# Performance work log

Measured on AMD Instinct MI355X. Metric: run time of the kernel, lower is better.

Reference implementation:

```python
import jax, jax.numpy as jnp
import numpy as np

N_NODES = 100000
N_EDGES = 1600000
N_GRAPHS = 64
VOCAB = 50000
D = 128
EPS = 1e-5


def setup_inputs() -> dict:
    key = jax.random.key(0)
    ks = jax.random.split(key, 24)
    tokens = jax.random.randint(ks[0], (N_NODES,), 0, VOCAB)
    src = jax.random.randint(ks[1], (N_EDGES,), 0, N_NODES)
    dst = jax.random.randint(ks[2], (N_EDGES,), 0, N_NODES)
    graph_ids = jnp.sort(jax.random.randint(ks[3], (N_NODES,), 0, N_GRAPHS))
    s = 1.0 / np.sqrt(D)
    inp = {
        'tokens': tokens, 'src': src, 'dst': dst, 'graph_ids': graph_ids,
        'embed': jax.random.normal(ks[4], (VOCAB, D), jnp.float32),
        'W1': jax.random.normal(ks[5], (D, D), jnp.float32) * s,
        'b1': jnp.zeros((D,), jnp.float32),
        'g1': jnp.ones((D,), jnp.float32), 'be1': jnp.zeros((D,), jnp.float32),
        'W2': jax.random.normal(ks[6], (D, D), jnp.float32) * s,
        'b2': jnp.zeros((D,), jnp.float32),
        'g2': jnp.ones((D,), jnp.float32), 'be2': jnp.zeros((D,), jnp.float32),
        'W3': jax.random.normal(ks[7], (D, D), jnp.float32) * s,
        'b3': jnp.zeros((D,), jnp.float32),
        'g3': jnp.ones((D,), jnp.float32), 'be3': jnp.zeros((D,), jnp.float32),
        'fcW1': jax.random.normal(ks[8], (D, D // 2), jnp.float32) * s,
        'fcb1': jnp.zeros((D // 2,), jnp.float32),
        'fcW2': jax.random.normal(ks[9], (D // 2, 2), jnp.float32) * (1.0 / np.sqrt(D // 2)),
        'fcb2': jnp.zeros((2,), jnp.float32),
    }
    return inp


def _graph_conv(h, src, dst, norm_src, norm_dst, W, b):
    # DGL GraphConv, norm='both': D_out^{-1/2} -> sum-aggregate -> D_in^{-1/2} -> linear
    msg = (h * norm_src[:, None])[src]                      # [E, D]
    agg = jax.ops.segment_sum(msg, dst, num_segments=N_NODES)
    return (agg * norm_dst[:, None]) @ W + b


def _bn_relu(h, gamma, beta):
    mu = jnp.mean(h, axis=0)
    var = jnp.mean((h - mu) ** 2, axis=0)                   # biased var (torch BN)
    return jax.nn.relu((h - mu) * jax.lax.rsqrt(var + EPS) * gamma + beta)


def reference(tokens, src, dst, graph_ids, embed,
              W1, b1, g1, be1, W2, b2, g2, be2, W3, b3, g3, be3,
              fcW1, fcb1, fcW2, fcb2):
    ones_e = jnp.ones((N_EDGES,), jnp.float32)
    deg_out = jnp.maximum(jax.ops.segment_sum(ones_e, src, num_segments=N_NODES), 1.0)
    deg_in = jnp.maximum(jax.ops.segment_sum(ones_e, dst, num_segments=N_NODES), 1.0)
    norm_src = jax.lax.rsqrt(deg_out)
    norm_dst = jax.lax.rsqrt(deg_in)

    h = embed[tokens]                                        # [N, D]
    h = _bn_relu(_graph_conv(h, src, dst, norm_src, norm_dst, W1, b1), g1, be1)
    h = _bn_relu(_graph_conv(h, src, dst, norm_src, norm_dst, W2, b2), g2, be2)
    h = _bn_relu(_graph_conv(h, src, dst, norm_src, norm_dst, W3, b3), g3, be3)

    # dgl.mean_nodes per graph
    sums = jax.ops.segment_sum(h, graph_ids, num_segments=N_GRAPHS)  # [G, D]
    cnts = jnp.maximum(jax.ops.segment_sum(jnp.ones((N_NODES,), jnp.float32), graph_ids, num_segments=N_GRAPHS), 1.0)
    hg = sums / cnts[:, None]

    hg = jax.nn.relu(hg @ fcW1 + fcb1)                       # dropout = identity (eval)
    return hg @ fcW2 + fcb2                                  # [G, 2]
```

## Files before the change

### kernel.cpp

```cpp
#include <hip/hip_runtime.h>

#define N_NODES 100000
#define N_EDGES 1600000
#define N_GRAPHS 64
#define DIM 128
#define BN_EPS 1e-5f
#define EPAD 2000000

#define NB_SENT 977
#define NB_WPREP 192
#define NB_HIST 391
#define NB_ZERO 40
#define NBUCK 782
#define NG (NBUCK * NB_HIST)
#define NB_SCANG 1195
#define BUCK_RESERVE 388

#define AT_STRIDE 136

typedef unsigned short ushort_t;
typedef unsigned char uchar_t;
typedef unsigned int uint_t;
typedef __attribute__((ext_vector_type(8))) short bf16x8;
typedef __attribute__((ext_vector_type(4))) float f32x4;

__device__ __forceinline__ float bfl(uint_t u) {
    union { uint_t i; float f; } v; v.i = u << 16; return v.f;
}
__device__ __forceinline__ float bfh(uint_t u) {
    union { uint_t i; float f; } v; v.i = u & 0xffff0000u; return v.f;
}
__device__ __forceinline__ ushort_t f2bf(float f) {
    union { float f; uint_t i; } v; v.f = f;
    uint_t x = v.i;
    return (ushort_t)((x + 0x7fffu + ((x >> 16) & 1u)) >> 16);
}
__device__ __forceinline__ uint_t pack2(float lo, float hi) {
    return ((uint_t)f2bf(hi) << 16) | (uint_t)f2bf(lo);
}

__global__ void k_front(const int* __restrict__ src, const int* __restrict__ dst,
                        ushort_t* __restrict__ bufA, int* __restrict__ esrc,
                        const float* __restrict__ w1, const float* __restrict__ w2,
                        const float* __restrict__ w3, ushort_t* __restrict__ wbt,
                        int* __restrict__ GG, int* __restrict__ deg,
                        int* __restrict__ zp, int zwords) {
    __shared__ int hh[NBUCK];
    int b = blockIdx.x;
    int t = threadIdx.x;
    if (b < NB_SENT) {
        int i0 = (b * 256 + t) * 8;
        int4 sv = make_int4(N_NODES, N_NODES, N_NODES, N_NODES);
        if (i0 + 8 <= EPAD) {
            *(int4*)(esrc + i0) = sv;
            *(int4*)(esrc + i0 + 4) = sv;
        } else {
            for (int i = i0; i < EPAD; ++i) esrc[i] = N_NODES;
        }
        if (b == 0 && t < 64)
            ((uint_t*)(bufA + (size_t)N_NODES * DIM))[t] = 0u;
        return;
    }
    b -= NB_SENT;
    if (b < NB_WPREP) {
        int i = b * 256 + t;
        int l = i >> 14;
        int idx = i & (DIM * DIM - 1);
        int n = idx >> 7, k = idx & (DIM - 1);
        const float* wsrc = (l == 0) ? w1 : (l == 1) ? w2 : w3;
        wbt[i] = f2bf(wsrc[k * DIM + n]);
        return;
    }
    b -= NB_WPREP;
    if (b < NB_HIST) {
        for (int k = t; k < NBUCK; k += 256) hh[k] = 0;
        __syncthreads();
        int e0 = b * 4096;
        int e1 = min(e0 + 4096, N_EDGES);
        for (int i = e0 + t; i < e1; i += 256) {
            atomicAdd(&hh[dst[i] >> 7], 1);
            atomicAdd(&deg[src[i]], 1);
        }
        __syncthreads();
        for (int k = t; k < NBUCK; k += 256)
            GG[k * NB_HIST + b] = hh[k];
        return;
    }
    b -= NB_HIST;
    {
        int i = b * 256 + t;
        if (i < zwords) zp[i] = 0;
    }
}

__global__ void k_scanA(const int* __restrict__ GG, int* __restrict__ Gs,
                        int* __restrict__ partials) {
    __shared__ int s[256];
    int t = threadIdx.x;
    int i = blockIdx.x * 256 + t;
    int v = (i < NG) ? GG[i] : 0;
    s[t] = v;
    __syncthreads();
    for (int off = 1; off < 256; off <<= 1) {
        int add = (t >= off) ? s[t - off] : 0;
        __syncthreads();
        s[t] += add;
        __syncthreads();
    }
    if (i < NG) Gs[i + 1] = s[t];
    if (t == 255) partials[blockIdx.x] = s[t];
}

__global__ void k_scanB(const int* __restrict__ partials, int* __restrict__ Gs) {
    __shared__ int s[256];
    int t = threadIdx.x;
    int p = 0;
    for (int j = t; j < (int)blockIdx.x; j += 256) p += partials[j];
    s[t] = p;
    __syncthreads();
    for (int off = 128; off > 0; off >>= 1) {
        if (t < off) s[t] += s[t + off];
        __syncthreads();
    }
    int prefix = s[0];
    int i = blockIdx.x * 256 + t;
    if (i < NG) Gs[i + 1] += prefix;
    if (blockIdx.x == 0 && t == 0) Gs[0] = 0;
}

__global__ void k_pass2(const int* __restrict__ src, const int* __restrict__ dst,
                        const int* __restrict__ Gs, uint_t* __restrict__ Cpk) {
    __shared__ int cur[NBUCK];
    int b = blockIdx.x;
    int t = threadIdx.x;
    for (int k = t; k < NBUCK; k += 256)
        cur[k] = Gs[k * NB_HIST + b];
    __syncthreads();
    int e0 = b * 4096;
    int e1 = min(e0 + 4096, N_EDGES);
    for (int i = e0 + t; i < e1; i += 256) {
        int d = dst[i];
        int s = src[i];
        int slot = atomicAdd(&cur[d >> 7], 1);
        Cpk[slot] = (uint_t)s | ((uint_t)(d & 127) << 17);
    }
}

__global__ void k_fine(const uint_t* __restrict__ Cpk, const int* __restrict__ Gs,
                       const int* __restrict__ deg,
                       const int* __restrict__ tokens, const float* __restrict__ embed,
                       int* __restrict__ esrc, int* __restrict__ rowptr,
                       int* __restrict__ pdeg, float* __restrict__ ns,
                       float* __restrict__ nd, ushort_t* __restrict__ bufA) {
    __shared__ int hcnt[128];
    __shared__ int hstart[128];
    __shared__ float lns[128];
    int k = blockIdx.x;
    int t = threadIdx.x;
    int node0 = k * 128;
    int nn = min(128, N_NODES - node0);
    int S = Gs[k * NB_HIST];
    int E = Gs[(k + 1) * NB_HIST];
    if (t < 128) hcnt[t] = 0;
    __syncthreads();
    for (int i = S + t; i < E; i += 256) atomicAdd(&hcnt[Cpk[i] >> 17], 1);
    __syncthreads();
    if (t == 0) {
        int acc = 0;
        for (int n = 0; n < nn; ++n) {
            hstart[n] = acc;
            acc += (hcnt[n] + 3) & ~3;
        }
    }
    __syncthreads();
    int base = (k * BUCK_RESERVE + S + 3) & ~3;
    if (t < nn) {
        int node = node0 + t;
        rowptr[node] = base + hstart[t];
        pdeg[node] = (hcnt[t] + 3) & ~3;
        nd[node] = rsqrtf(fmaxf((float)hcnt[t], 1.0f));
        float v = rsqrtf(fmaxf((float)deg[node], 1.0f));
        ns[node] = v;
        lns[t] = v;
    }
    if (k == 0 && t == 0) ns[N_NODES] = 0.f;
    __syncthreads();
    for (int i = S + t; i < E; i += 256) {
        uint_t pk = Cpk[i];
        int slot = atomicAdd(&hstart[pk >> 17], 1);
        esrc[base + slot] = (int)(pk & 0x1FFFFu);
    }
    for (int slot = t; slot < nn * 16; slot += 256) {
        int nloc = slot >> 4, sub = slot & 15;
        int node = node0 + nloc;
        float s = lns[nloc];
        const float* ep = embed + (size_t)tokens[node] * DIM + sub * 8;
        float4 a = *(const float4*)ep;
        float4 c = *(const float4*)(ep + 4);
        uint4 o;
        o.x = pack2(a.x * s, a.y * s);
        o.y = pack2(a.z * s, a.w * s);
        o.z = pack2(c.x * s, c.y * s);
        o.w = pack2(c.z * s, c.w * s);
        *(uint4*)(bufA + (size_t)node * DIM + sub * 8) = o;
    }
}

__global__ void k_prescale(const ushort_t* __restrict__ yin, const float* __restrict__ ns,
                           const float* __restrict__ bnsum, const float* __restrict__ bnsq,
                           const float* __restrict__ g, const float* __restrict__ be,
                           ushort_t* __restrict__ xout) {
    __shared__ float sa[DIM], sc[DIM];
    int t = threadIdx.x;
    if (t < DIM) {
        float mu = bnsum[t] * (1.0f / N_NODES);
        float var = bnsq[t] * (1.0f / N_NODES) - mu * mu;
        float rstd = rsqrtf(var + BN_EPS);
        float a = g[t] * rstd;
        sa[t] = a;
        sc[t] = be[t] - mu * a;
    }
    __syncthreads();
    int gid = blockIdx.x * 256 + t;
    int node = gid >> 4, sub = gid & 15;
    float s = ns[node];
    uint4 u = *(const uint4*)(yin + (size_t)node * DIM + sub * 8);
    float v[8] = {bfl(u.x), bfh(u.x), bfl(u.y), bfh(u.y),
                  bfl(u.z), bfh(u.z), bfl(u.w), bfh(u.w)};
    const float* a = sa + sub * 8;
    const float* c = sc + sub * 8;
#pragma unroll
    for (int i = 0; i < 8; ++i) v[i] = fmaxf(fmaf(v[i], a[i], c[i]), 0.f) * s;
    uint4 o;
    o.x = pack2(v[0], v[1]); o.y = pack2(v[2], v[3]);
    o.z = pack2(v[4], v[5]); o.w = pack2(v[6], v[7]);
    *(uint4*)(xout + (size_t)node * DIM + sub * 8) = o;
}

__global__ __launch_bounds__(256) void k_agggemm(const ushort_t* __restrict__ hs,
        const int* __restrict__ rowptr, const int* __restrict__ pdeg,
        const int* __restrict__ esrc, const float* __restrict__ nd,
        const ushort_t* __restrict__ wbt, const float* __restrict__ bias,
        ushort_t* __restrict__ y,
        float* __restrict__ bnsum, float* __restrict__ bnsq) {
    __shared__ ushort_t at[64 * AT_STRIDE];
    __shared__ float csum[DIM], csq[DIM];
    int tid = threadIdx.x;
    int wave = tid >> 6;
    int lane = tid & 63;
    if (tid < DIM) { csum[tid] = 0.f; csq[tid] = 0.f; }
    __syncthreads();

    int bnode = blockIdx.x * 64 + wave * 16;
    int quad = lane >> 4;
    int m16 = lane & 15;

    const ushort_t* hrow = hs + (size_t)m16 * 8;

    int rpv = 0, epv = 0;
    float ndv = 0.f;
    if (lane < 16) {
        int nnode = bnode + lane;
        if (nnode < N_NODES) {
            rpv = rowptr[nnode];
            epv = rpv + pdeg[nnode];
            ndv = nd[nnode];
        }
    }
    int ws = __shfl(rpv, 0);
    int T = (__shfl(epv, 15) - ws) >> 2;

#define FEATLD(ix) (*(const uint4*)(hrow + (size_t)(ix) * DIM))
#define ACCU(F)                                                     \
    {                                                               \
        a[0] += bfl((F).x); a[1] += bfh((F).x);                     \
        a[2] += bfl((F).y); a[3] += bfh((F).y);                     \
        a[4] += bfl((F).z); a[5] += bfh((F).z);                     \
        a[6] += bfl((F).w); a[7] += bfh((F).w);                     \
    }
#define FLUSH()                                                     \
    {                                                               \
        float nv = __shfl(ndv, ni);                                 \
        _Pragma("unroll")                                           \
        for (int j = 0; j < 8; ++j) {                               \
            a[j] += __shfl_xor(a[j], 16);                           \
            a[j] += __shfl_xor(a[j], 32);                           \
        }                                                           \
        if (quad == 0) {                                            \
            uint4 o;                                                \
            o.x = pack2(a[0] * nv, a[1] * nv);                      \
            o.y = pack2(a[2] * nv, a[3] * nv);                      \
            o.z = pack2(a[4] * nv, a[5] * nv);                      \
            o.w = pack2(a[6] * nv, a[7] * nv);                      \
            *(uint4*)&at[(wave * 16 + ni) * AT_STRIDE + m16 * 8] = o; \
        }                                                           \
        _Pragma("unroll")                                           \
        for (int j = 0; j < 8; ++j) a[j] = 0.f;                     \
    }
#define BCHK()                                                      \
    while (ni < 16 && pos >= end_cur) {                             \
        FLUSH();                                                    \
        ++ni;                                                       \
        end_cur = __shfl(epv, ni < 16 ? ni : 15);                   \
    }

    float a[8] = {0.f, 0.f, 0.f, 0.f, 0.f, 0.f, 0.f, 0.f};
    int ni = 0;
    int end_cur = __shfl(epv, 0);
    int pos = ws + 4;

    int sl = ws + quad;
    int i0 = esrc[sl], i1 = esrc[sl + 4], i2 = esrc[sl + 8], i3 = esrc[sl + 12];
    uint4 f0 = FEATLD(i0), f1 = FEATLD(i1), f2 = FEATLD(i2), f3 = FEATLD(i3);
    i0 = esrc[sl + 16]; i1 = esrc[sl + 20]; i2 = esrc[sl + 24]; i3 = esrc[sl + 28];
    sl += 32;

    int t = 0;
    for (; t + 4 <= T; t += 4) {
        { int n_ = esrc[sl]; sl += 4; ACCU(f0); f0 = FEATLD(i0); i0 = n_; BCHK(); pos += 4; }
        { int n_ = esrc[sl]; sl += 4; ACCU(f1); f1 = FEATLD(i1); i1 = n_; BCHK(); pos += 4; }
        { int n_ = esrc[sl]; sl += 4; ACCU(f2); f2 = FEATLD(i2); i2 = n_; BCHK(); pos += 4; }
        { int n_ = esrc[sl]; sl += 4; ACCU(f3); f3 = FEATLD(i3); i3 = n_; BCHK(); pos += 4; }
    }
    if (t + 0 < T) { ACCU(f0); BCHK(); pos += 4; }
    if (t + 1 < T) { ACCU(f1); BCHK(); pos += 4; }
    if (t + 2 < T) { ACCU(f2); BCHK(); pos += 4; }
    while (ni < 16) { FLUSH(); ++ni; }
#undef BCHK
#undef FLUSH
#undef ACCU
#undef FEATLD

    f32x4 acc[8];
#pragma unroll
    for (int nb = 0; nb < 8; ++nb) acc[nb] = (f32x4)(0.f);

    const ushort_t* ap = &at[(wave * 16 + m16) * AT_STRIDE + quad * 8];
#pragma unroll
    for (int k0b = 0; k0b < 4; ++k0b) {
        bf16x8 af = *(const bf16x8*)(ap + k0b * 32);
#pragma unroll
        for (int nb = 0; nb < 8; ++nb) {
            int ncol = nb * 16 + m16;
            bf16x8 bfg = *(const bf16x8*)(wbt + (size_t)ncol * DIM + k0b * 32 + quad * 8);
            acc[nb] = __builtin_amdgcn_mfma_f32_16x16x32_bf16(af, bfg, acc[nb], 0, 0, 0);
        }
    }

#pragma unroll
    for (int nb = 0; nb < 8; ++nb) {
        int col = nb * 16 + m16;
        float bcol = bias[col];
        float ps = 0.f, pq = 0.f;
#pragma unroll
        for (int reg = 0; reg < 4; ++reg) {
            int r = bnode + quad * 4 + reg;
            if (r < N_NODES) {
                float v = acc[nb][reg] + bcol;
                ps += v; pq += v * v;
                y[(size_t)r * DIM + col] = f2bf(v);
            }
        }
        atomicAdd(&csum[col], ps);
        atomicAdd(&csq[col], pq);
    }
    __syncthreads();
    if (tid < DIM) {
        atomicAdd(&bnsum[tid], csum[tid]);
        atomicAdd(&bnsq[tid], csq[tid]);
    }
}

#define POOL_NODES 128
__global__ void k_pool(const ushort_t* __restrict__ yin, const int* __restrict__ gids,
                       const float* __restrict__ bnsum, const float* __restrict__ bnsq,
                       const float* __restrict__ g, const float* __restrict__ be,
                       float* __restrict__ pool, int* __restrict__ cnt) {
    __shared__ int h[N_GRAPHS];
    int col = threadIdx.x;
    float mu = bnsum[col] * (1.0f / N_NODES);
    float var = bnsq[col] * (1.0f / N_NODES) - mu * mu;
    float rstd = rsqrtf(var + BN_EPS);
    float a = g[col] * rstd;
    float c = be[col] - mu * a;
    if (col < N_GRAPHS) h[col] = 0;
    __syncthreads();
    int base = blockIdx.x * POOL_NODES;
    int end = min(base + POOL_NODES, N_NODES);
    for (int n = base + col; n < end; n += 128) atomicAdd(&h[gids[n]], 1);
    __syncthreads();
    if (col < N_GRAPHS && h[col]) atomicAdd(&cnt[col], h[col]);
    float acc = 0.f;
    int cur = gids[base];
    for (int n = base; n < end; ++n) {
        int gg = gids[n];
        if (gg != cur) {
            atomicAdd(&pool[(size_t)cur * DIM + col], acc);
            acc = 0.f;
            cur = gg;
        }
        uint_t u = *(const uint_t*)(yin + (size_t)n * DIM + (col & ~1));
        float v = (col & 1) ? bfh(u) : bfl(u);
        acc += fmaxf(fmaf(v, a, c), 0.f);
    }
    atomicAdd(&pool[(size_t)cur * DIM + col], acc);
}

__global__ void k_final(const float* __restrict__ pool, const int* __restrict__ cnt,
                        const float* __restrict__ fcW1, const float* __restrict__ fcb1,
                        const float* __restrict__ fcW2, const float* __restrict__ fcb2,
                        float* __restrict__ out) {
    __shared__ float hg[DIM];
    __shared__ float z[64];
    int g = blockIdx.x;
    int t = threadIdx.x;
    float cf = fmaxf((float)cnt[g], 1.0f);
    hg[t] = pool[(size_t)g * DIM + t] / cf;
    __syncthreads();
    if (t < 64) {
        float acc = fcb1[t];
        for (int k = 0; k < DIM; ++k)
            acc += hg[k] * fcW1[k * 64 + t];
        z[t] = fmaxf(acc, 0.f);
    }
    __syncthreads();
    if (t < 2) {
        float acc = fcb2[t];
        for (int k = 0; k < 64; ++k)
            acc += z[k] * fcW2[k * 2 + t];
        out[g * 2 + t] = acc;
    }
}

extern "C" void kernel_launch(void* const* d_in, const int* in_sizes, int n_in,
                              void* d_out, int out_size, void* d_ws, size_t ws_size,
                              hipStream_t stream) {
    const int* tokens = (const int*)d_in[0];
    const int* src = (const int*)d_in[1];
    const int* dst = (const int*)d_in[2];
    const int* gids = (const int*)d_in[3];
    const float* embed = (const float*)d_in[4];
    const float* W1 = (const float*)d_in[5];
    const float* b1 = (const float*)d_in[6];
    const float* g1 = (const float*)d_in[7];
    const float* be1 = (const float*)d_in[8];
    const float* W2 = (const float*)d_in[9];
    const float* b2 = (const float*)d_in[10];
    const float* g2 = (const float*)d_in[11];
    const float* be2 = (const float*)d_in[12];
    const float* W3 = (const float*)d_in[13];
    const float* b3 = (const float*)d_in[14];
    const float* g3 = (const float*)d_in[15];
    const float* be3 = (const float*)d_in[16];
    const float* fcW1 = (const float*)d_in[17];
    const float* fcb1 = (const float*)d_in[18];
    const float* fcW2 = (const float*)d_in[19];
    const float* fcb2 = (const float*)d_in[20];
    float* out = (float*)d_out;

    char* w = (char*)d_ws;
    auto alloc = [&](size_t bytes) {
        void* p = (void*)w;
        w += (bytes + 255) & ~(size_t)255;
        return p;
    };
    ushort_t* bufH = (ushort_t*)alloc((size_t)(N_NODES + 1) * DIM * 2);
    ushort_t* bufA = (ushort_t*)alloc((size_t)(N_NODES + 1) * DIM * 2);
    ushort_t* bufY = (ushort_t*)alloc((size_t)(N_NODES + 1) * DIM * 2);
    int* esrc = (int*)alloc((size_t)EPAD * 4);
    int* rowptr = (int*)alloc((size_t)N_NODES * 4);
    int* pdeg = (int*)alloc((size_t)N_NODES * 4);
    float* ns = (float*)alloc((size_t)(N_NODES + 1) * 4);
    float* nd = (float*)alloc((size_t)N_NODES * 4);
    int* deg = (int*)alloc((size_t)N_NODES * 4);
    ushort_t* wbt = (ushort_t*)alloc(3 * DIM * DIM * 2);
    int* GG = (int*)alloc((size_t)NG * 4);
    int* Gs = (int*)alloc((size_t)(NG + 1) * 4);
    int* partials = (int*)alloc(4096 * 4);
    uint_t* Cpk = (uint_t*)alloc((size_t)N_EDGES * 4);
    char* zstart = w;
    float* bnsum = (float*)alloc(3 * DIM * 4);
    float* bnsq = (float*)alloc(3 * DIM * 4);
    float* pool = (float*)alloc((size_t)N_GRAPHS * DIM * 4);
    int* cnt = (int*)alloc((size_t)N_GRAPHS * 4);
    int zwords = (int)((size_t)(w - zstart) / 4);

    hipMemsetAsync(deg, 0, (size_t)N_NODES * 4, stream);
    k_front<<<NB_SENT + NB_WPREP + NB_HIST + NB_ZERO, 256, 0, stream>>>(
        src, dst, bufA, esrc, W1, W2, W3, wbt, GG, deg, (int*)zstart, zwords);
    k_scanA<<<NB_SCANG, 256, 0, stream>>>(GG, Gs, partials);
    k_scanB<<<NB_SCANG, 256, 0, stream>>>(partials, Gs);
    k_pass2<<<NB_HIST, 256, 0, stream>>>(src, dst, Gs, Cpk);
    k_fine<<<NBUCK, 256, 0, stream>>>(Cpk, Gs, deg, tokens, embed,
                                      esrc, rowptr, pdeg, ns, nd, bufA);

    int nb_fused = (N_NODES + 63) / 64;
    int nb_ps = 6250;

    k_agggemm<<<nb_fused, 256, 0, stream>>>(bufA, rowptr, pdeg, esrc, nd,
                                            wbt, b1, bufY, bnsum, bnsq);
    k_prescale<<<nb_ps, 256, 0, stream>>>(bufY, ns, bnsum, bnsq, g1, be1, bufA);
    k_agggemm<<<nb_fused, 256, 0, stream>>>(bufA, rowptr, pdeg, esrc, nd,
                                            wbt + (size_t)DIM * DIM, b2, bufH,
                                            bnsum + DIM, bnsq + DIM);
    k_prescale<<<nb_ps, 256, 0, stream>>>(bufH, ns, bnsum + DIM, bnsq + DIM, g2, be2, bufA);
    k_agggemm<<<nb_fused, 256, 0, stream>>>(bufA, rowptr, pdeg, esrc, nd,
                                            wbt + (size_t)2 * DIM * DIM, b3, bufY,
                                            bnsum + 2 * DIM, bnsq + 2 * DIM);

    k_pool<<<(N_NODES + POOL_NODES - 1) / POOL_NODES, DIM, 0, stream>>>(
        bufY, gids, bnsum + 2 * DIM, bnsq + 2 * DIM, g3, be3, pool, cnt);
    k_final<<<N_GRAPHS, DIM, 0, stream>>>(pool, cnt, fcW1, fcb1, fcW2, fcb2, out);
}
```

Baseline: 636.2 us.

## Replace two-level bucketed CSR build with direct per-node degree scan and atomic scatter

The CSR construction drops the bucket histogram, the large bucket scan, the packed intermediate pass and the fine per-bucket sort. It now counts in-degree with global atomics, scans padded per-node degrees directly, and scatters source ids with per-node global atomic cursors. The embedding gather is fused into the same launch as the scatter. This removes a kernel launch and the intermediate buffer, but it relies on heavy global atomics on random destinations. Edge order within a row becomes nondeterministic, and the esrc writes lose the locality the bucketed approach had.

```diff
diff --git a/kernel.cpp b/kernel.cpp
--- a/kernel.cpp
+++ b/kernel.cpp
@@ -9,17 +9,14 @@
 
 #define NB_SENT 977
 #define NB_WPREP 192
-#define NB_HIST 391
+#define NB_EDGE 391
 #define NB_ZERO 40
-#define NBUCK 782
-#define NG (NBUCK * NB_HIST)
-#define NB_SCANG 1195
-#define BUCK_RESERVE 388
+#define NB_SCAN 391
+#define NB_EMB 782
 
 #define AT_STRIDE 136
 
 typedef unsigned short ushort_t;
-typedef unsigned char uchar_t;
 typedef unsigned int uint_t;
 typedef __attribute__((ext_vector_type(8))) short bf16x8;
 typedef __attribute__((ext_vector_type(4))) float f32x4;
@@ -43,9 +40,8 @@
                         ushort_t* __restrict__ bufA, int* __restrict__ esrc,
                         const float* __restrict__ w1, const float* __restrict__ w2,
                         const float* __restrict__ w3, ushort_t* __restrict__ wbt,
-                        int* __restrict__ GG, int* __restrict__ deg,
+                        int* __restrict__ indeg, int* __restrict__ outdeg,
                         int* __restrict__ zp, int zwords) {
-    __shared__ int hh[NBUCK];
     int b = blockIdx.x;
     int t = threadIdx.x;
     if (b < NB_SENT) {
@@ -72,33 +68,28 @@
         return;
     }
     b -= NB_WPREP;
-    if (b < NB_HIST) {
-        for (int k = t; k < NBUCK; k += 256) hh[k] = 0;
-        __syncthreads();
+    if (b < NB_EDGE) {
         int e0 = b * 4096;
         int e1 = min(e0 + 4096, N_EDGES);
         for (int i = e0 + t; i < e1; i += 256) {
-            atomicAdd(&hh[dst[i] >> 7], 1);
-            atomicAdd(&deg[src[i]], 1);
-        }
-        __syncthreads();
-        for (int k = t; k < NBUCK; k += 256)
-            GG[k * NB_HIST + b] = hh[k];
+            atomicAdd(&outdeg[src[i]], 1);
+            atomicAdd(&indeg[dst[i]], 1);
+        }
         return;
     }
-    b -= NB_HIST;
+    b -= NB_EDGE;
     {
         int i = b * 256 + t;
         if (i < zwords) zp[i] = 0;
     }
 }
 
-__global__ void k_scanA(const int* __restrict__ GG, int* __restrict__ Gs,
-                        int* __restrict__ partials) {
+__global__ void k_scanA(const int* __restrict__ indeg, int* __restrict__ rowptr,
+                        int* __restrict__ pdeg, int* __restrict__ partials) {
     __shared__ int s[256];
     int t = threadIdx.x;
     int i = blockIdx.x * 256 + t;
-    int v = (i < NG) ? GG[i] : 0;
+    int v = (i < N_NODES) ? ((indeg[i] + 3) & ~3) : 0;
     s[t] = v;
     __syncthreads();
     for (int off = 1; off < 256; off <<= 1) {
@@ -107,11 +98,17 @@
         s[t] += add;
         __syncthreads();
     }
-    if (i < NG) Gs[i + 1] = s[t];
+    if (i < N_NODES) {
+        rowptr[i] = s[t] - v;
+        pdeg[i] = v;
+    }
     if (t == 255) partials[blockIdx.x] = s[t];
 }
 
-__global__ void k_scanB(const int* __restrict__ partials, int* __restrict__ Gs) {
+__global__ void k_scanB(const int* __restrict__ partials, const int* __restrict__ indeg,
+                        const int* __restrict__ outdeg, int* __restrict__ rowptr,
+                        int* __restrict__ cur, float* __restrict__ nd,
+                        float* __restrict__ ns) {
     __shared__ int s[256];
     int t = threadIdx.x;
     int p = 0;
@@ -124,72 +121,37 @@
     }
     int prefix = s[0];
     int i = blockIdx.x * 256 + t;
-    if (i < NG) Gs[i + 1] += prefix;
-    if (blockIdx.x == 0 && t == 0) Gs[0] = 0;
-}
-
-__global__ void k_pass2(const int* __restrict__ src, const int* __restrict__ dst,
-                        const int* __restrict__ Gs, uint_t* __restrict__ Cpk) {
-    __shared__ int cur[NBUCK];
+    if (i < N_NODES) {
+        int rp = rowptr[i] + prefix;
+        rowptr[i] = rp;
+        cur[i] = rp;
+        nd[i] = rsqrtf(fmaxf((float)indeg[i], 1.0f));
+        ns[i] = rsqrtf(fmaxf((float)outdeg[i], 1.0f));
+    }
+    if (blockIdx.x == 0 && t == 0) ns[N_NODES] = 0.f;
+}
+
+__global__ void k_scat(const int* __restrict__ src, const int* __restrict__ dst,
+                       int* __restrict__ cur, int* __restrict__ esrc,
+                       const int* __restrict__ tokens, const float* __restrict__ embed,
+                       const float* __restrict__ ns, ushort_t* __restrict__ bufA) {
+    __shared__ float lns[128];
     int b = blockIdx.x;
     int t = threadIdx.x;
-    for (int k = t; k < NBUCK; k += 256)
-        cur[k] = Gs[k * NB_HIST + b];
-    __syncthreads();
-    int e0 = b * 4096;
-    int e1 = min(e0 + 4096, N_EDGES);
-    for (int i = e0 + t; i < e1; i += 256) {
-        int d = dst[i];
-        int s = src[i];
-        int slot = atomicAdd(&cur[d >> 7], 1);
-        Cpk[slot] = (uint_t)s | ((uint_t)(d & 127) << 17);
-    }
-}
-
-__global__ void k_fine(const uint_t* __restrict__ Cpk, const int* __restrict__ Gs,
-                       const int* __restrict__ deg,
-                       const int* __restrict__ tokens, const float* __restrict__ embed,
-                       int* __restrict__ esrc, int* __restrict__ rowptr,
-                       int* __restrict__ pdeg, float* __restrict__ ns,
-                       float* __restrict__ nd, ushort_t* __restrict__ bufA) {
-    __shared__ int hcnt[128];
-    __shared__ int hstart[128];
-    __shared__ float lns[128];
-    int k = blockIdx.x;
-    int t = threadIdx.x;
-    int node0 = k * 128;
+    if (b < NB_EDGE) {
+        int e0 = b * 4096;
+        int e1 = min(e0 + 4096, N_EDGES);
+        for (int i = e0 + t; i < e1; i += 256) {
+            int slot = atomicAdd(&cur[dst[i]], 1);
+            esrc[slot] = src[i];
+        }
+        return;
+    }
+    b -= NB_EDGE;
+    int node0 = b * 128;
     int nn = min(128, N_NODES - node0);
-    int S = Gs[k * NB_HIST];
-    int E = Gs[(k + 1) * NB_HIST];
-    if (t < 128) hcnt[t] = 0;
-    __syncthreads();
-    for (int i = S + t; i < E; i += 256) atomicAdd(&hcnt[Cpk[i] >> 17], 1);
-    __syncthreads();
-    if (t == 0) {
-        int acc = 0;
-        for (int n = 0; n < nn; ++n) {
-            hstart[n] = acc;
-            acc += (hcnt[n] + 3) & ~3;
-        }
-    }
-    __syncthreads();
-    int base = (k * BUCK_RESERVE + S + 3) & ~3;
-    if (t < nn) {
-        int node = node0 + t;
-        rowptr[node] = base + hstart[t];
-        pdeg[node] = (hcnt[t] + 3) & ~3;
-        nd[node] = rsqrtf(fmaxf((float)hcnt[t], 1.0f));
-        float v = rsqrtf(fmaxf((float)deg[node], 1.0f));
-        ns[node] = v;
-        lns[t] = v;
-    }
-    if (k == 0 && t == 0) ns[N_NODES] = 0.f;
-    __syncthreads();
-    for (int i = S + t; i < E; i += 256) {
-        uint_t pk = Cpk[i];
-        int slot = atomicAdd(&hstart[pk >> 17], 1);
-        esrc[base + slot] = (int)(pk & 0x1FFFFu);
-    }
+    if (t < nn) lns[t] = ns[node0 + t];
+    __syncthreads();
     for (int slot = t; slot < nn * 16; slot += 256) {
         int nloc = slot >> 4, sub = slot & 15;
         int node = node0 + nloc;
@@ -472,12 +434,12 @@
     int* pdeg = (int*)alloc((size_t)N_NODES * 4);
     float* ns = (float*)alloc((size_t)(N_NODES + 1) * 4);
     float* nd = (float*)alloc((size_t)N_NODES * 4);
-    int* deg = (int*)alloc((size_t)N_NODES * 4);
+    int* degio = (int*)alloc((size_t)2 * N_NODES * 4);
+    int* indeg = degio;
+    int* outdeg = degio + N_NODES;
+    int* cur = (int*)alloc((size_t)N_NODES * 4);
     ushort_t* wbt = (ushort_t*)alloc(3 * DIM * DIM * 2);
-    int* GG = (int*)alloc((size_t)NG * 4);
-    int* Gs = (int*)alloc((size_t)(NG + 1) * 4);
     int* partials = (int*)alloc(4096 * 4);
-    uint_t* Cpk = (uint_t*)alloc((size_t)N_EDGES * 4);
     char* zstart = w;
     float* bnsum = (float*)alloc(3 * DIM * 4);
     float* bnsq = (float*)alloc(3 * DIM * 4);
@@ -485,14 +447,13 @@
     int* cnt = (int*)alloc((size_t)N_GRAPHS * 4);
     int zwords = (int)((size_t)(w - zstart) / 4);
 
-    hipMemsetAsync(deg, 0, (size_t)N_NODES * 4, stream);
-    k_front<<<NB_SENT + NB_WPREP + NB_HIST + NB_ZERO, 256, 0, stream>>>(
-        src, dst, bufA, esrc, W1, W2, W3, wbt, GG, deg, (int*)zstart, zwords);
-    k_scanA<<<NB_SCANG, 256, 0, stream>>>(GG, Gs, partials);
-    k_scanB<<<NB_SCANG, 256, 0, stream>>>(partials, Gs);
-    k_pass2<<<NB_HIST, 256, 0, stream>>>(src, dst, Gs, Cpk);
-    k_fine<<<NBUCK, 256, 0, stream>>>(Cpk, Gs, deg, tokens, embed,
-                                      esrc, rowptr, pdeg, ns, nd, bufA);
+    hipMemsetAsync(degio, 0, (size_t)2 * N_NODES * 4, stream);
+    k_front<<<NB_SENT + NB_WPREP + NB_EDGE + NB_ZERO, 256, 0, stream>>>(
+        src, dst, bufA, esrc, W1, W2, W3, wbt, indeg, outdeg, (int*)zstart, zwords);
+    k_scanA<<<NB_SCAN, 256, 0, stream>>>(indeg, rowptr, pdeg, partials);
+    k_scanB<<<NB_SCAN, 256, 0, stream>>>(partials, indeg, outdeg, rowptr, cur, nd, ns);
+    k_scat<<<NB_EDGE + NB_EMB, 256, 0, stream>>>(src, dst, cur, esrc,
+                                                 tokens, embed, ns, bufA);
 
     int nb_fused = (N_NODES + 63) / 64;
     int nb_ps = 6250;
```

Result: slower. 724.4 us (+13.9%).
